# Kernel optimization log

Hardware: AMD Instinct MI355X
Metric: run time of the kernel (lower is better)

## Reference

```python
import jax, jax.numpy as jnp
import numpy as np

N = 50000        # nodes
E = 1600000      # edges (avg degree 32)
DIM_IN = 128
H = 4            # num_heads
D1 = 100         # gc1 per-head out dim
D2 = 20          # gc2 per-head out dim
B = 64           # graphs in the batch
EPS = 1e-5
SLOPE = 0.01     # torch leaky_relu default


def setup_inputs() -> dict:
    key = jax.random.key(0)
    ks = jax.random.split(key, 16)
    sc = lambda fan: 1.0 / np.sqrt(fan)
    inp = {
        'feat': jax.random.normal(ks[0], (N, DIM_IN), jnp.float32),
        'src': jax.random.randint(ks[1], (E,), 0, N, jnp.int32),
        'dst': jax.random.randint(ks[2], (E,), 0, N, jnp.int32),
        'graph_id': jnp.sort(jax.random.randint(ks[3], (N,), 0, B, jnp.int32)),
        # GAT layer 1: per-head fc weight [H, din, dout], attn vector [H, 2*dout]
        'W1': jax.random.normal(ks[4], (H, DIM_IN, D1), jnp.float32) * sc(DIM_IN),
        'a1': jax.random.normal(ks[5], (H, 2 * D1), jnp.float32) * sc(2 * D1),
        # GAT layer 2 (input is cat of heads: H*D1 = 400)
        'W2': jax.random.normal(ks[6], (H, H * D1, D2), jnp.float32) * sc(H * D1),
        'a2': jax.random.normal(ks[7], (H, 2 * D2), jnp.float32) * sc(2 * D2),
        # readout MLP 20 -> 128 -> 32 -> 1
        'Wf1': jax.random.normal(ks[8], (D2, 128), jnp.float32) * sc(D2),
        'bf1': jnp.zeros((128,), jnp.float32),
        'Wf2': jax.random.normal(ks[9], (128, 32), jnp.float32) * sc(128),
        'bf2': jnp.zeros((32,), jnp.float32),
        'Wf3': jax.random.normal(ks[10], (32, 1), jnp.float32) * sc(32),
        'bf3': jnp.zeros((1,), jnp.float32),
        'gamma2': jnp.ones((32,), jnp.float32),   # bn2 weight
        'beta2': jnp.zeros((32,), jnp.float32),   # bn2 bias
    }
    return inp


def _gat_heads(h, W, a, src, dst):
    """Per-head GAT: gather-attn -> segment softmax over dst mailboxes -> scatter-sum.
    Returns list of [N, dout] head outputs. Loop over H=4 heads (small fixed set)."""
    outs = []
    for i in range(W.shape[0]):
        z = h @ W[i]                               # [N, dout]
        d = z.shape[1]
        s_src = z @ a[i, :d]                       # [N] (attn split: a.[z_src,z_dst])
        s_dst = z @ a[i, d:]                       # [N]
        e = jax.nn.leaky_relu(s_src[src] + s_dst[dst], SLOPE)   # [E]
        m = jax.ops.segment_max(e, dst, num_segments=N)          # stable softmax max
        ex = jnp.exp(e - m[dst])
        den = jax.ops.segment_sum(ex, dst, num_segments=N)
        alpha = ex / den[dst]                      # [E] segment softmax
        outs.append(jax.ops.segment_sum(alpha[:, None] * z[src], dst, num_segments=N))
    return outs


def reference(feat, src, dst, graph_id, W1, a1, W2, a2,
              Wf1, bf1, Wf2, bf2, Wf3, bf3, gamma2, beta2):
    src = src.astype(jnp.int32); dst = dst.astype(jnp.int32)
    h = jax.nn.relu(jnp.concatenate(_gat_heads(feat, W1, a1, src, dst), axis=1))  # [N,400]
    h = jax.nn.relu(jnp.mean(jnp.stack(_gat_heads(h, W2, a2, src, dst), 0), 0))   # [N,20]
    # dgl.mean_nodes: per-graph mean of node features
    counts = jax.ops.segment_sum(jnp.ones((N,), h.dtype), graph_id, num_segments=B)
    hg = jax.ops.segment_sum(h, graph_id, num_segments=B) / counts[:, None]        # [B,20]
    out = jax.nn.relu(hg @ Wf1 + bf1)              # dropout = identity (eval)
    out = out @ Wf2 + bf2                          # [B,32]
    mu = jnp.mean(out, axis=0)                     # BatchNorm1d (training stats, biased var)
    var = jnp.mean((out - mu) ** 2, axis=0)
    out = jax.nn.relu(gamma2 * (out - mu) * jax.lax.rsqrt(var + EPS) + beta2)
    return out @ Wf3 + bf3                         # [B,1]
```

## Files before the change

### kernel.cpp

```cpp
#include <hip/hip_runtime.h>
#include <hip/hip_bf16.h>
#include <math.h>

#define N_NODES 50000
#define N_EDGES 1600000
#define DIN 128
#define NH 4
#define D1 100
#define D2 20
#define NB 64
#define EPS_BN 1e-5f


typedef unsigned int uint;
typedef unsigned short ushort;
typedef short short8v __attribute__((ext_vector_type(8)));
typedef float float4v __attribute__((ext_vector_type(4)));

#define Z1_ROWU 208
#define Z1_HU 52
#define Z2_ROWU 64

__device__ __forceinline__ void bf16x2_unpack(uint p, float& lo, float& hi) {
  lo = __uint_as_float(p << 16);
  hi = __uint_as_float(p & 0xffff0000u);
}

__device__ __forceinline__ ushort f2bf(float f) {
  uint u = __float_as_uint(f);
  return (ushort)((u + 0x7fffu + ((u >> 16) & 1u)) >> 16);
}

__global__ void prep_b1t(const float* __restrict__ W1, ushort* __restrict__ B1t) {
  int o = blockIdx.x * 256 + threadIdx.x;
  int h = o >> 14;
  int r = o & 16383;
  int j = r >> 7, k = r & 127;
  float v = (j < D1) ? W1[((size_t)h * DIN + k) * D1 + j] : 0.f;
  B1t[o] = f2bf(v);
}

__global__ void prep_b2t(const float* __restrict__ W2, ushort* __restrict__ B2t) {
  int idx = blockIdx.x * 256 + threadIdx.x;
  if (idx >= 80 * 416) return;
  int c = idx / 416, k = idx - c * 416;
  int h = c / D2, j = c - h * D2;
  float v = (k < NH * D1) ? W2[((size_t)h * (NH * D1) + k) * D2 + j] : 0.f;
  B2t[idx] = f2bf(v);
}

__global__ __launch_bounds__(256) void gemm1_mfma(const float* __restrict__ feat,
                                                  const ushort* __restrict__ B1t,
                                                  const float* __restrict__ a1,
                                                  ushort* __restrict__ z1b,
                                                  float* __restrict__ ssrc,
                                                  float* __restrict__ sdst) {
  __shared__ __align__(16) short Bs[128 * 136];
  __shared__ float asd[2][104];
  const int row0 = blockIdx.x * 128;
  const int h = blockIdx.y;
  const int tid = threadIdx.x;
  {
    const uint* bsrc = reinterpret_cast<const uint*>(B1t + (size_t)h * 16384);
#pragma unroll
    for (int it = 0; it < 32; it++) {
      int idx = tid + it * 256;
      int j = idx >> 6, kk = idx & 63;
      *reinterpret_cast<uint*>(&Bs[j * 136 + kk * 2]) = bsrc[idx];
    }
  }
  if (tid < 208) {
    int which = tid >= 104;
    int cl = which ? tid - 104 : tid;
    asd[which][cl] = (cl < D1) ? a1[h * 2 * D1 + which * D1 + cl] : 0.f;
  }
  const int wv = tid >> 6, lane = tid & 63;
  const int m = lane & 15, q = lane >> 4;
  short8v a[2][4];
#pragma unroll
  for (int mt = 0; mt < 2; mt++) {
    int row = row0 + wv * 32 + mt * 16 + m;
    bool ok = row < N_NODES;
    const float* fr = feat + (size_t)(ok ? row : 0) * DIN;
#pragma unroll
    for (int kq = 0; kq < 4; kq++) {
      short8v s = (short8v){0, 0, 0, 0, 0, 0, 0, 0};
      if (ok) {
        float4 v0 = *reinterpret_cast<const float4*>(fr + kq * 32 + q * 8);
        float4 v1 = *reinterpret_cast<const float4*>(fr + kq * 32 + q * 8 + 4);
        s[0] = (short)f2bf(v0.x); s[1] = (short)f2bf(v0.y);
        s[2] = (short)f2bf(v0.z); s[3] = (short)f2bf(v0.w);
        s[4] = (short)f2bf(v1.x); s[5] = (short)f2bf(v1.y);
        s[6] = (short)f2bf(v1.z); s[7] = (short)f2bf(v1.w);
      }
      a[mt][kq] = s;
    }
  }
  __syncthreads();
  float4v acc[2][8];
#pragma unroll
  for (int mt = 0; mt < 2; mt++)
#pragma unroll
    for (int t = 0; t < 8; t++) acc[mt][t] = (float4v){0.f, 0.f, 0.f, 0.f};
#pragma unroll
  for (int kq = 0; kq < 4; kq++) {
#pragma unroll
    for (int t = 0; t < 8; t++) {
      short8v b = *reinterpret_cast<const short8v*>(&Bs[(t * 16 + m) * 136 + kq * 32 + q * 8]);
      acc[0][t] = __builtin_amdgcn_mfma_f32_16x16x32_bf16(a[0][kq], b, acc[0][t], 0, 0, 0);
      acc[1][t] = __builtin_amdgcn_mfma_f32_16x16x32_bf16(a[1][kq], b, acc[1][t], 0, 0, 0);
    }
  }
#pragma unroll
  for (int mt = 0; mt < 2; mt++) {
#pragma unroll
    for (int t = 0; t < 8; t++) {
      int cl = t * 16 + m;
      if (cl < 104) {
#pragma unroll
        for (int reg = 0; reg < 4; reg++) {
          int row = row0 + wv * 32 + mt * 16 + q * 4 + reg;
          if (row < N_NODES)
            z1b[(size_t)row * 416 + h * 104 + cl] = (cl < D1) ? f2bf(acc[mt][t][reg]) : (ushort)0;
        }
      }
    }
  }
  float aws[8], awd[8];
#pragma unroll
  for (int t = 0; t < 8; t++) {
    aws[t] = asd[0][t * 16 + m];
    awd[t] = asd[1][t * 16 + m];
  }
  float s1[2][4], s2v[2][4];
#pragma unroll
  for (int mt = 0; mt < 2; mt++)
#pragma unroll
    for (int reg = 0; reg < 4; reg++) {
      float p1 = 0.f, p2 = 0.f;
#pragma unroll
      for (int t = 0; t < 8; t++) {
        p1 += acc[mt][t][reg] * aws[t];
        p2 += acc[mt][t][reg] * awd[t];
      }
      s1[mt][reg] = p1;
      s2v[mt][reg] = p2;
    }
#pragma unroll
  for (int mt = 0; mt < 2; mt++)
#pragma unroll
    for (int reg = 0; reg < 4; reg++) {
#pragma unroll
      for (int off = 8; off >= 1; off >>= 1) {
        s1[mt][reg] += __shfl_xor(s1[mt][reg], off);
        s2v[mt][reg] += __shfl_xor(s2v[mt][reg], off);
      }
    }
  if (m == 0) {
#pragma unroll
    for (int mt = 0; mt < 2; mt++)
#pragma unroll
      for (int reg = 0; reg < 4; reg++) {
        int row = row0 + wv * 32 + mt * 16 + q * 4 + reg;
        if (row < N_NODES) ssrc[h * N_NODES + row] = s1[mt][reg];
      }
  } else if (m == 1) {
#pragma unroll
    for (int mt = 0; mt < 2; mt++)
#pragma unroll
      for (int reg = 0; reg < 4; reg++) {
        int row = row0 + wv * 32 + mt * 16 + q * 4 + reg;
        if (row < N_NODES) sdst[h * N_NODES + row] = s2v[mt][reg];
      }
  }
}

__global__ __launch_bounds__(256) void gemm2_mfma(const ushort* __restrict__ h1b,
                                                  const ushort* __restrict__ B2t,
                                                  const float* __restrict__ a2,
                                                  ushort* __restrict__ z2b,
                                                  float* __restrict__ ssrc,
                                                  float* __restrict__ sdst) {
  __shared__ __align__(16) short As[64 * 40];
  __shared__ __align__(16) short Bs[80 * 40];
  __shared__ float awcol[2][4][80];
  const int row0 = blockIdx.x * 64;
  const int tid = threadIdx.x;
  const int wv = tid >> 6, lane = tid & 63;
  const int m = lane & 15, q = lane >> 4;
  const uint* au = reinterpret_cast<const uint*>(h1b);
  const uint* bu = reinterpret_cast<const uint*>(B2t);
  uint* asu = reinterpret_cast<uint*>(As);
  uint* bsu = reinterpret_cast<uint*>(Bs);
  for (int i = tid; i < 640; i += 256) {
    int sc = i / 320;
    int r = i - sc * 320;
    int hh = r / 80, col = r - hh * 80;
    int ch = col / 20;
    awcol[sc][hh][col] = (ch == hh) ? a2[hh * 2 * D2 + sc * D2 + (col - 20 * hh)] : 0.f;
  }
  float4v acc[5];
#pragma unroll
  for (int t = 0; t < 5; t++) acc[t] = (float4v){0.f, 0.f, 0.f, 0.f};
  for (int ch = 0; ch < 13; ch++) {
    int k0u = ch * 16;
    {
      int idx = tid;
#pragma unroll
      for (int it = 0; it < 4; it++, idx += 256) {
        int r = idx >> 4, ku = idx & 15;
        int row = row0 + r;
        uint v = 0;
        if (row < N_NODES && (k0u + ku) < 200) v = au[(size_t)row * 200 + k0u + ku];
        asu[r * 20 + ku] = v;
      }
      idx = tid;
#pragma unroll
      for (int it = 0; it < 5; it++, idx += 256) {
        int c = idx >> 4, ku = idx & 15;
        bsu[c * 20 + ku] = bu[(size_t)c * 208 + k0u + ku];
      }
    }
    __syncthreads();
    short8v a = *reinterpret_cast<const short8v*>(&As[(wv * 16 + m) * 40 + q * 8]);
#pragma unroll
    for (int t = 0; t < 5; t++) {
      short8v b = *reinterpret_cast<const short8v*>(&Bs[(t * 16 + m) * 40 + q * 8]);
      acc[t] = __builtin_amdgcn_mfma_f32_16x16x32_bf16(a, b, acc[t], 0, 0, 0);
    }
    __syncthreads();
  }
#pragma unroll
  for (int t = 0; t < 5; t++) {
    int col = t * 16 + m;
#pragma unroll
    for (int reg = 0; reg < 4; reg++) {
      int row = row0 + wv * 16 + q * 4 + reg;
      if (row < N_NODES) z2b[(size_t)row * 128 + col] = f2bf(acc[t][reg]);
    }
  }
  float w1v[4][5], w2v[4][5];
#pragma unroll
  for (int hh = 0; hh < 4; hh++)
#pragma unroll
    for (int t = 0; t < 5; t++) {
      w1v[hh][t] = awcol[0][hh][t * 16 + m];
      w2v[hh][t] = awcol[1][hh][t * 16 + m];
    }
  float ps[2][4][4];
#pragma unroll
  for (int hh = 0; hh < 4; hh++)
#pragma unroll
    for (int reg = 0; reg < 4; reg++) {
      float p1 = 0.f, p2 = 0.f;
#pragma unroll
      for (int t = 0; t < 5; t++) {
        p1 += acc[t][reg] * w1v[hh][t];
        p2 += acc[t][reg] * w2v[hh][t];
      }
      ps[0][hh][reg] = p1;
      ps[1][hh][reg] = p2;
    }
#pragma unroll
  for (int hh = 0; hh < 4; hh++)
#pragma unroll
    for (int reg = 0; reg < 4; reg++) {
#pragma unroll
      for (int off = 8; off >= 1; off >>= 1) {
        ps[0][hh][reg] += __shfl_xor(ps[0][hh][reg], off);
        ps[1][hh][reg] += __shfl_xor(ps[1][hh][reg], off);
      }
    }
#pragma unroll
  for (int hh = 0; hh < 4; hh++) {
    if (m == hh) {
#pragma unroll
      for (int reg = 0; reg < 4; reg++) {
        int row = row0 + wv * 16 + q * 4 + reg;
        if (row < N_NODES) ssrc[hh * N_NODES + row] = ps[0][hh][reg];
      }
    }
    if (m == hh + 4) {
#pragma unroll
      for (int reg = 0; reg < 4; reg++) {
        int row = row0 + wv * 16 + q * 4 + reg;
        if (row < N_NODES) sdst[hh * N_NODES + row] = ps[1][hh][reg];
      }
    }
  }
}

__global__ void hist_kernel(const int* __restrict__ dst, int* __restrict__ cnt,
                            int* __restrict__ rank) {
  int e = blockIdx.x * blockDim.x + threadIdx.x;
  if (e < N_EDGES) rank[e] = atomicAdd(&cnt[dst[e]], 1);
}

__global__ __launch_bounds__(512) void scan1_kernel(const int* __restrict__ cnt,
                                                    int* __restrict__ row_ptr,
                                                    int* __restrict__ btot, int n) {
  __shared__ int ws[8];
  int b = blockIdx.x, tid = threadIdx.x, lane = tid & 63, wv = tid >> 6;
  int i = b * 512 + tid;
  int v = (i < n) ? cnt[i] : 0;
  int orig = v;
  for (int off = 1; off < 64; off <<= 1) {
    int t = __shfl_up(v, off);
    if (lane >= off) v += t;
  }
  if (lane == 63) ws[wv] = v;
  __syncthreads();
  int wo = 0;
  for (int j = 0; j < wv; j++) wo += ws[j];
  if (i < n) row_ptr[i] = wo + v - orig;
  if (tid == 511) btot[b] = wo + v;
}

__global__ __launch_bounds__(128) void scan2_kernel(int* __restrict__ btot,
                                                    int* __restrict__ row_ptr_n, int nb) {
  __shared__ int ws2[2];
  int tid = threadIdx.x, lane = tid & 63, wv = tid >> 6;
  int v = (tid < nb) ? btot[tid] : 0;
  int orig = v;
  for (int off = 1; off < 64; off <<= 1) {
    int t = __shfl_up(v, off);
    if (lane >= off) v += t;
  }
  if (lane == 63) ws2[wv] = v;
  __syncthreads();
  int wo = (wv == 1) ? ws2[0] : 0;
  if (tid < nb) btot[tid] = wo + v - orig;
  if (tid == nb - 1) *row_ptr_n = wo + v;
}

__global__ __launch_bounds__(512) void scan3_kernel(int* __restrict__ row_ptr,
                                                    const int* __restrict__ btot, int n) {
  int i = blockIdx.x * 512 + threadIdx.x;
  if (i < n) row_ptr[i] += btot[blockIdx.x];
}

__global__ void fill_kernel(const int* __restrict__ src, const int* __restrict__ dst,
                            const int* __restrict__ row_ptr, const int* __restrict__ rank,
                            int* __restrict__ csr_src) {
  int e = blockIdx.x * blockDim.x + threadIdx.x;
  if (e < N_EDGES) csr_src[row_ptr[dst[e]] + rank[e]] = src[e];
}

__global__ __launch_bounds__(256) void agg1_kernel(const ushort* __restrict__ z,
                                                   const float* __restrict__ ssrc,
                                                   const float* __restrict__ sdst,
                                                   const int* __restrict__ row_ptr,
                                                   const int* __restrict__ csr_src,
                                                   ushort* __restrict__ h1b) {
  __shared__ float lw[NH][128];
  const int d = blockIdx.x;
  const int h = threadIdx.x >> 6, lane = threadIdx.x & 63;
  const int beg = row_ptr[d], end = row_ptr[d + 1];
  const int deg = end - beg;
  uint* h1u = reinterpret_cast<uint*>(h1b);
  const size_t ou = (size_t)d * 200 + h * 50 + lane;
  const bool act = lane < D1 / 2;
  if (deg == 0) {
    if (act) h1u[ou] = 0u;
    return;
  }
  const int hN = h * N_NODES;
  const float sd = sdst[hN + d];
  const uint* zb = reinterpret_cast<const uint*>(z);
  const int hco = h * Z1_HU + lane;
  float den = 0.f;
  float aE0 = 0.f, aE1 = 0.f, aE2 = 0.f, aE3 = 0.f;
  float aO0 = 0.f, aO1 = 0.f, aO2 = 0.f, aO3 = 0.f;
  for (int c0 = 0; c0 < deg; c0 += 128) {
    const int cn = min(128, deg - c0);
    const int cb = beg + c0;
    for (int i = lane; i < cn; i += 64) {
      int s = csr_src[cb + i];
      float e = ssrc[hN + s] + sd;
      e = fmaxf(e, 0.01f * e);
      float x = __expf(e);
      lw[h][i] = x;
      den += x;
    }
    if (act) {
      int j = 0;
      for (; j + 8 <= cn; j += 8) {
        int s0 = csr_src[cb + j + 0], s1 = csr_src[cb + j + 1];
        int s2 = csr_src[cb + j + 2], s3 = csr_src[cb + j + 3];
        int s4 = csr_src[cb + j + 4], s5 = csr_src[cb + j + 5];
        int s6 = csr_src[cb + j + 6], s7 = csr_src[cb + j + 7];
        float x0 = lw[h][j + 0], x1 = lw[h][j + 1];
        float x2 = lw[h][j + 2], x3 = lw[h][j + 3];
        float x4 = lw[h][j + 4], x5 = lw[h][j + 5];
        float x6 = lw[h][j + 6], x7 = lw[h][j + 7];
        uint p0 = zb[(size_t)s0 * Z1_ROWU + hco];
        uint p1 = zb[(size_t)s1 * Z1_ROWU + hco];
        uint p2 = zb[(size_t)s2 * Z1_ROWU + hco];
        uint p3 = zb[(size_t)s3 * Z1_ROWU + hco];
        uint p4 = zb[(size_t)s4 * Z1_ROWU + hco];
        uint p5 = zb[(size_t)s5 * Z1_ROWU + hco];
        uint p6 = zb[(size_t)s6 * Z1_ROWU + hco];
        uint p7 = zb[(size_t)s7 * Z1_ROWU + hco];
        float lo, hi;
        bf16x2_unpack(p0, lo, hi); aE0 += x0 * lo; aO0 += x0 * hi;
        bf16x2_unpack(p1, lo, hi); aE1 += x1 * lo; aO1 += x1 * hi;
        bf16x2_unpack(p2, lo, hi); aE2 += x2 * lo; aO2 += x2 * hi;
        bf16x2_unpack(p3, lo, hi); aE3 += x3 * lo; aO3 += x3 * hi;
        bf16x2_unpack(p4, lo, hi); aE0 += x4 * lo; aO0 += x4 * hi;
        bf16x2_unpack(p5, lo, hi); aE1 += x5 * lo; aO1 += x5 * hi;
        bf16x2_unpack(p6, lo, hi); aE2 += x6 * lo; aO2 += x6 * hi;
        bf16x2_unpack(p7, lo, hi); aE3 += x7 * lo; aO3 += x7 * hi;
      }
      for (; j < cn; j++) {
        int s = csr_src[cb + j];
        float x = lw[h][j];
        uint p = zb[(size_t)s * Z1_ROWU + hco];
        float lo, hi;
        bf16x2_unpack(p, lo, hi);
        aE0 += x * lo;
        aO0 += x * hi;
      }
    }
  }
#pragma unroll
  for (int off = 32; off > 0; off >>= 1) den += __shfl_xor(den, off);
  if (!act) return;
  float inv = 1.0f / den;
  float vE = ((aE0 + aE1) + (aE2 + aE3)) * inv;
  float vO = ((aO0 + aO1) + (aO2 + aO3)) * inv;
  vE = vE > 0.f ? vE : 0.f;
  vO = vO > 0.f ? vO : 0.f;
  h1u[ou] = (uint)f2bf(vE) | ((uint)f2bf(vO) << 16);
}

__global__ __launch_bounds__(256) void agg2_kernel(const ushort* __restrict__ z,
                                                   const float* __restrict__ ssrc,
                                                   const float* __restrict__ sdst,
                                                   const int* __restrict__ row_ptr,
                                                   const int* __restrict__ csr_src,
                                                   float* __restrict__ h2) {
  __shared__ float xw[4][8][4];
  __shared__ int sw[4][8];
  __shared__ float accb[4][40][2];
  __shared__ float denb[4][4];
  const int d = blockIdx.x;
  const int wv = threadIdx.x >> 6, lane = threadIdx.x & 63;
  const int beg = row_ptr[d];
  const int deg = row_ptr[d + 1] - beg;
  if (deg == 0) {
    if (threadIdx.x < D2) h2[(size_t)d * D2 + threadIdx.x] = 0.f;
    return;
  }
  const int eh_h = lane & 3, eh_e = lane >> 2;
  const int hq = lane / 10;
  const uint* zu = reinterpret_cast<const uint*>(z);
  float sd = 0.f;
  if (lane < 32) sd = sdst[eh_h * N_NODES + d];
  float den = 0.f;
  float acc0 = 0.f, acc1 = 0.f;
  for (int c0 = wv * 8; c0 < deg; c0 += 32) {
    const int cn = min(8, deg - c0);
    const int cb = beg + c0;
    if (lane < 32) {
      int ee = (eh_e < cn) ? eh_e : 0;
      int s = csr_src[cb + ee];
      float e = ssrc[eh_h * N_NODES + s] + sd;
      e = fmaxf(e, 0.01f * e);
      float x = (eh_e < cn) ? __expf(e) : 0.f;
      den += x;
      xw[wv][eh_e][eh_h] = x;
      if (eh_h == 0) sw[wv][eh_e] = s;
    }
    if (lane < 40) {
#pragma unroll
      for (int e = 0; e < 8; e++) {
        int se = sw[wv][e];
        float xx = xw[wv][e][hq];
        uint p = zu[(size_t)se * Z2_ROWU + lane];
        float lo, hi;
        bf16x2_unpack(p, lo, hi);
        acc0 += xx * lo;
        acc1 += xx * hi;
      }
    }
  }
  den += __shfl_xor(den, 4);
  den += __shfl_xor(den, 8);
  den += __shfl_xor(den, 16);
  if (lane < 4) denb[wv][lane] = den;
  if (lane < 40) {
    accb[wv][lane][0] = acc0;
    accb[wv][lane][1] = acc1;
  }
  __syncthreads();
  if (threadIdx.x < 10) {
    int j = threadIdx.x;
    float vE = 0.f, vO = 0.f;
#pragma unroll
    for (int h = 0; h < 4; h++) {
      float dn = denb[0][h] + denb[1][h] + denb[2][h] + denb[3][h];
      float invd = 1.0f / dn;
      int sl = h * 10 + j;
      float lo = accb[0][sl][0] + accb[1][sl][0] + accb[2][sl][0] + accb[3][sl][0];
      float hi = accb[0][sl][1] + accb[1][sl][1] + accb[2][sl][1] + accb[3][sl][1];
      vE += lo * invd;
      vO += hi * invd;
    }
    vE *= 0.25f;
    vO *= 0.25f;
    h2[(size_t)d * D2 + 2 * j] = vE > 0.f ? vE : 0.f;
    h2[(size_t)d * D2 + 2 * j + 1] = vO > 0.f ? vO : 0.f;
  }
}

__global__ __launch_bounds__(256) void pool_kernel(const float* __restrict__ h2,
                                                   const int* __restrict__ gid,
                                                   float* __restrict__ hg,
                                                   int* __restrict__ gcnt) {
  int wave = threadIdx.x >> 6, lane = threadIdx.x & 63;
  int n = (blockIdx.x * 4 + wave) * 64 + lane;
  bool valid = n < N_NODES;
  int g = gid[valid ? n : (N_NODES - 1)];
  int g0 = __shfl(g, 0), g63 = __shfl(g, 63);
  unsigned long long mask = __ballot(valid);
  if (g0 == g63) {
    if (lane == 0) atomicAdd(&gcnt[g0], (int)__popcll(mask));
#pragma unroll
    for (int c = 0; c < D2; c++) {
      float v = valid ? h2[(size_t)n * D2 + c] : 0.f;
#pragma unroll
      for (int off = 32; off > 0; off >>= 1) v += __shfl_xor(v, off);
      if (lane == 0) atomicAdd(&hg[g0 * D2 + c], v);
    }
  } else if (valid) {
    atomicAdd(&gcnt[g], 1);
    for (int c = 0; c < D2; c++) atomicAdd(&hg[g * D2 + c], h2[(size_t)n * D2 + c]);
  }
}

__global__ __launch_bounds__(256) void head_kernel(const float* __restrict__ hg,
                                                   const int* __restrict__ gcnt,
                                                   const float* __restrict__ Wf1,
                                                   const float* __restrict__ bf1,
                                                   const float* __restrict__ Wf2,
                                                   const float* __restrict__ bf2,
                                                   const float* __restrict__ Wf3,
                                                   const float* __restrict__ bf3,
                                                   const float* __restrict__ gamma,
                                                   const float* __restrict__ beta,
                                                   float* __restrict__ out) {
  __shared__ float X[NB][D2];
  __shared__ float T1[NB][128];
  __shared__ float T2[NB][32];
  __shared__ float scale_s[32], shift_s[32];
  int tid = threadIdx.x;
  for (int i = tid; i < NB * D2; i += 256) {
    int r = i / D2, c = i % D2;
    X[r][c] = hg[i] / (float)gcnt[r];
  }
  __syncthreads();
  for (int i = tid; i < NB * 128; i += 256) {
    int r = i >> 7, c = i & 127;
    float s = bf1[c];
#pragma unroll
    for (int k = 0; k < D2; k++) s += X[r][k] * Wf1[k * 128 + c];
    T1[r][c] = s > 0.f ? s : 0.f;
  }
  __syncthreads();
  for (int i = tid; i < NB * 32; i += 256) {
    int r = i >> 5, c = i & 31;
    float s = bf2[c];
#pragma unroll
    for (int k = 0; k < 128; k++) s += T1[r][k] * Wf2[k * 32 + c];
    T2[r][c] = s;
  }
  __syncthreads();
  if (tid < 32) {
    float mu = 0.f;
    for (int r = 0; r < NB; r++) mu += T2[r][tid];
    mu *= (1.f / NB);
    float var = 0.f;
    for (int r = 0; r < NB; r++) {
      float dv = T2[r][tid] - mu;
      var += dv * dv;
    }
    var *= (1.f / NB);
    float sc = gamma[tid] * rsqrtf(var + EPS_BN);
    scale_s[tid] = sc;
    shift_s[tid] = beta[tid] - mu * sc;
  }
  __syncthreads();
  if (tid < NB) {
    float s = bf3[0];
#pragma unroll
    for (int c = 0; c < 32; c++) {
      float y = scale_s[c] * T2[tid][c] + shift_s[c];
      y = y > 0.f ? y : 0.f;
      s += y * Wf3[c];
    }
    out[tid] = s;
  }
}


extern "C" void kernel_launch(void* const* d_in, const int* in_sizes, int n_in,
                              void* d_out, int out_size, void* d_ws, size_t ws_size,
                              hipStream_t stream) {
  const float* feat = (const float*)d_in[0];
  const int* src = (const int*)d_in[1];
  const int* dst = (const int*)d_in[2];
  const int* gid = (const int*)d_in[3];
  const float* W1 = (const float*)d_in[4];
  const float* a1 = (const float*)d_in[5];
  const float* W2 = (const float*)d_in[6];
  const float* a2 = (const float*)d_in[7];
  const float* Wf1 = (const float*)d_in[8];
  const float* bf1 = (const float*)d_in[9];
  const float* Wf2 = (const float*)d_in[10];
  const float* bf2 = (const float*)d_in[11];
  const float* Wf3 = (const float*)d_in[12];
  const float* bf3 = (const float*)d_in[13];
  const float* gamma2 = (const float*)d_in[14];
  const float* beta2 = (const float*)d_in[15];
  float* outp = (float*)d_out;

  char* p = (char*)d_ws;
  auto alloc = [&](size_t bytes) {
    void* q = (void*)p;
    p += (bytes + 255) & ~(size_t)255;
    return q;
  };
  ushort* z1b = (ushort*)alloc((size_t)N_NODES * 416 * 2);
  ushort* z2b = (ushort*)alloc((size_t)N_NODES * 128 * 2);
  ushort* h1b = (ushort*)alloc((size_t)N_NODES * NH * D1 * 2);
  float* h2 = (float*)alloc((size_t)N_NODES * D2 * 4);
  float* ssrc = (float*)alloc((size_t)NH * N_NODES * 4);
  float* sdst = (float*)alloc((size_t)NH * N_NODES * 4);
  int* cnt = (int*)alloc((size_t)N_NODES * 4);
  int* row_ptr = (int*)alloc((size_t)(N_NODES + 1) * 4);
  int* rank = (int*)alloc((size_t)N_EDGES * 4);
  int* csr = (int*)alloc((size_t)N_EDGES * 4);
  int* btot = (int*)alloc((size_t)128 * 4);
  ushort* B1t = (ushort*)alloc((size_t)NH * 128 * 128 * 2);
  ushort* B2t = (ushort*)alloc((size_t)80 * 416 * 2);
  float* hg = (float*)alloc((size_t)NB * D2 * 4);
  int* gcnt = (int*)alloc((size_t)NB * 4);

  const int rows128 = (N_NODES + 127) / 128;
  const int rows64 = (N_NODES + 63) / 64;
  const int eblk = (N_EDGES + 255) / 256;
  const int nblk = (N_NODES + 255) / 256;
  const int sblk = (N_NODES + 511) / 512;

  hipMemsetAsync(cnt, 0, (size_t)N_NODES * 4, stream);
  hist_kernel<<<eblk, 256, 0, stream>>>(dst, cnt, rank);
  scan1_kernel<<<sblk, 512, 0, stream>>>(cnt, row_ptr, btot, N_NODES);
  scan2_kernel<<<1, 128, 0, stream>>>(btot, row_ptr + N_NODES, sblk);
  scan3_kernel<<<sblk, 512, 0, stream>>>(row_ptr, btot, N_NODES);
  fill_kernel<<<eblk, 256, 0, stream>>>(src, dst, row_ptr, rank, csr);

  prep_b1t<<<256, 256, 0, stream>>>(W1, B1t);
  prep_b2t<<<130, 256, 0, stream>>>(W2, B2t);

  gemm1_mfma<<<dim3(rows128, NH), 256, 0, stream>>>(feat, B1t, a1, z1b, ssrc, sdst);
  agg1_kernel<<<N_NODES, 256, 0, stream>>>(z1b, ssrc, sdst, row_ptr, csr, h1b);

  gemm2_mfma<<<rows64, 256, 0, stream>>>(h1b, B2t, a2, z2b, ssrc, sdst);
  agg2_kernel<<<N_NODES, 256, 0, stream>>>(z2b, ssrc, sdst, row_ptr, csr, h2);

  hipMemsetAsync(hg, 0, (size_t)NB * D2 * 4, stream);
  hipMemsetAsync(gcnt, 0, (size_t)NB * 4, stream);
  pool_kernel<<<nblk, 256, 0, stream>>>(h2, gid, hg, gcnt);
  head_kernel<<<1, 256, 0, stream>>>(hg, gcnt, Wf1, bf1, Wf2, bf2, Wf3, bf3,
                                     gamma2, beta2, outp);
}
```

Baseline: 615.8 us.

## Map one wave per node in agg2 and stage full W2 tile in gemm2

agg2 now gives each destination node to a single wavefront rather than a 256-thread block. Cross-lane shuffles replace the shared-memory staging and the block-wide barrier-based reduction, which should cut idle waves and synchronisation for low-degree nodes. gemm2 loads each wave's A rows straight into registers with vector loads and stages the whole B matrix (about 64KB) in LDS once, removing the per-chunk barriers. The large LDS footprint may lower gemm2 occupancy, and the row-strided B reads in LDS may cause bank conflicts.

```diff
diff --git a/kernel.cpp b/kernel.cpp
--- a/kernel.cpp
+++ b/kernel.cpp
@@ -16,6 +16,7 @@
 typedef unsigned short ushort;
 typedef short short8v __attribute__((ext_vector_type(8)));
 typedef float float4v __attribute__((ext_vector_type(4)));
+typedef uint uint4v __attribute__((ext_vector_type(4)));
 
 #define Z1_ROWU 208
 #define Z1_HU 52
@@ -181,8 +182,7 @@
                                                   ushort* __restrict__ z2b,
                                                   float* __restrict__ ssrc,
                                                   float* __restrict__ sdst) {
-  __shared__ __align__(16) short As[64 * 40];
-  __shared__ __align__(16) short Bs[80 * 40];
+  __shared__ __align__(16) short Bs[80 * 400 + 16];
   __shared__ float awcol[2][4][80];
   const int row0 = blockIdx.x * 64;
   const int tid = threadIdx.x;
@@ -190,8 +190,22 @@
   const int m = lane & 15, q = lane >> 4;
   const uint* au = reinterpret_cast<const uint*>(h1b);
   const uint* bu = reinterpret_cast<const uint*>(B2t);
-  uint* asu = reinterpret_cast<uint*>(As);
   uint* bsu = reinterpret_cast<uint*>(Bs);
+  const int row = row0 + wv * 16 + m;
+  const bool rok = row < N_NODES;
+  uint4v a_all[13];
+#pragma unroll
+  for (int ch = 0; ch < 13; ch++) {
+    int k0 = ch * 16 + q * 4;
+    uint4v v = (uint4v){0u, 0u, 0u, 0u};
+    if (rok && (k0 + 4 <= 200)) v = *reinterpret_cast<const uint4v*>(au + (size_t)row * 200 + k0);
+    a_all[ch] = v;
+  }
+  for (int i = tid; i < 16000; i += 256) {
+    int c = i / 200, k = i - c * 200;
+    bsu[c * 200 + k] = bu[(size_t)c * 208 + k];
+  }
+  if (tid < 8) bsu[16000 + tid] = 0u;
   for (int i = tid; i < 640; i += 256) {
     int sc = i / 320;
     int r = i - sc * 320;
@@ -199,44 +213,26 @@
     int ch = col / 20;
     awcol[sc][hh][col] = (ch == hh) ? a2[hh * 2 * D2 + sc * D2 + (col - 20 * hh)] : 0.f;
   }
+  __syncthreads();
   float4v acc[5];
 #pragma unroll
   for (int t = 0; t < 5; t++) acc[t] = (float4v){0.f, 0.f, 0.f, 0.f};
+#pragma unroll
   for (int ch = 0; ch < 13; ch++) {
-    int k0u = ch * 16;
-    {
-      int idx = tid;
-#pragma unroll
-      for (int it = 0; it < 4; it++, idx += 256) {
-        int r = idx >> 4, ku = idx & 15;
-        int row = row0 + r;
-        uint v = 0;
-        if (row < N_NODES && (k0u + ku) < 200) v = au[(size_t)row * 200 + k0u + ku];
-        asu[r * 20 + ku] = v;
-      }
-      idx = tid;
-#pragma unroll
-      for (int it = 0; it < 5; it++, idx += 256) {
-        int c = idx >> 4, ku = idx & 15;
-        bsu[c * 20 + ku] = bu[(size_t)c * 208 + k0u + ku];
-      }
-    }
-    __syncthreads();
-    short8v a = *reinterpret_cast<const short8v*>(&As[(wv * 16 + m) * 40 + q * 8]);
+    short8v a = *reinterpret_cast<const short8v*>(&a_all[ch]);
 #pragma unroll
     for (int t = 0; t < 5; t++) {
-      short8v b = *reinterpret_cast<const short8v*>(&Bs[(t * 16 + m) * 40 + q * 8]);
+      short8v b = *reinterpret_cast<const short8v*>(&Bs[(t * 16 + m) * 400 + ch * 32 + q * 8]);
       acc[t] = __builtin_amdgcn_mfma_f32_16x16x32_bf16(a, b, acc[t], 0, 0, 0);
     }
-    __syncthreads();
   }
 #pragma unroll
   for (int t = 0; t < 5; t++) {
     int col = t * 16 + m;
 #pragma unroll
     for (int reg = 0; reg < 4; reg++) {
-      int row = row0 + wv * 16 + q * 4 + reg;
-      if (row < N_NODES) z2b[(size_t)row * 128 + col] = f2bf(acc[t][reg]);
+      int r2 = row0 + wv * 16 + q * 4 + reg;
+      if (r2 < N_NODES) z2b[(size_t)r2 * 128 + col] = f2bf(acc[t][reg]);
     }
   }
   float w1v[4][5], w2v[4][5];
@@ -276,15 +272,15 @@
     if (m == hh) {
 #pragma unroll
       for (int reg = 0; reg < 4; reg++) {
-        int row = row0 + wv * 16 + q * 4 + reg;
-        if (row < N_NODES) ssrc[hh * N_NODES + row] = ps[0][hh][reg];
+        int r2 = row0 + wv * 16 + q * 4 + reg;
+        if (r2 < N_NODES) ssrc[hh * N_NODES + r2] = ps[0][hh][reg];
       }
     }
     if (m == hh + 4) {
 #pragma unroll
       for (int reg = 0; reg < 4; reg++) {
-        int row = row0 + wv * 16 + q * 4 + reg;
-        if (row < N_NODES) sdst[hh * N_NODES + row] = ps[1][hh][reg];
+        int r2 = row0 + wv * 16 + q * 4 + reg;
+        if (r2 < N_NODES) sdst[hh * N_NODES + r2] = ps[1][hh][reg];
       }
     }
   }
@@ -439,46 +435,44 @@
                                                    const int* __restrict__ row_ptr,
                                                    const int* __restrict__ csr_src,
                                                    float* __restrict__ h2) {
-  __shared__ float xw[4][8][4];
-  __shared__ int sw[4][8];
-  __shared__ float accb[4][40][2];
-  __shared__ float denb[4][4];
-  const int d = blockIdx.x;
   const int wv = threadIdx.x >> 6, lane = threadIdx.x & 63;
+  const int d = blockIdx.x * 4 + wv;
+  if (d >= N_NODES) return;
   const int beg = row_ptr[d];
   const int deg = row_ptr[d + 1] - beg;
   if (deg == 0) {
-    if (threadIdx.x < D2) h2[(size_t)d * D2 + threadIdx.x] = 0.f;
+    if (lane < 10) {
+      h2[(size_t)d * D2 + 2 * lane] = 0.f;
+      h2[(size_t)d * D2 + 2 * lane + 1] = 0.f;
+    }
     return;
   }
   const int eh_h = lane & 3, eh_e = lane >> 2;
   const int hq = lane / 10;
   const uint* zu = reinterpret_cast<const uint*>(z);
-  float sd = 0.f;
-  if (lane < 32) sd = sdst[eh_h * N_NODES + d];
-  float den = 0.f;
-  float acc0 = 0.f, acc1 = 0.f;
-  for (int c0 = wv * 8; c0 < deg; c0 += 32) {
+  const float sd = (lane < 32) ? sdst[eh_h * N_NODES + d] : 0.f;
+  float den = 0.f, acc0 = 0.f, acc1 = 0.f;
+  for (int c0 = 0; c0 < deg; c0 += 8) {
     const int cn = min(8, deg - c0);
     const int cb = beg + c0;
+    float x = 0.f;
+    int s = 0;
     if (lane < 32) {
       int ee = (eh_e < cn) ? eh_e : 0;
-      int s = csr_src[cb + ee];
+      s = csr_src[cb + ee];
       float e = ssrc[eh_h * N_NODES + s] + sd;
       e = fmaxf(e, 0.01f * e);
-      float x = (eh_e < cn) ? __expf(e) : 0.f;
+      x = (eh_e < cn) ? __expf(e) : 0.f;
       den += x;
-      xw[wv][eh_e][eh_h] = x;
-      if (eh_h == 0) sw[wv][eh_e] = s;
-    }
-    if (lane < 40) {
-#pragma unroll
-      for (int e = 0; e < 8; e++) {
-        int se = sw[wv][e];
-        float xx = xw[wv][e][hq];
-        uint p = zu[(size_t)se * Z2_ROWU + lane];
+    }
+#pragma unroll
+    for (int e = 0; e < 8; e++) {
+      float xx = __shfl(x, e * 4 + hq);
+      int se = __shfl(s, e * 4);
+      if (lane < 40) {
+        uint pd = zu[(size_t)se * Z2_ROWU + lane];
         float lo, hi;
-        bf16x2_unpack(p, lo, hi);
+        bf16x2_unpack(pd, lo, hi);
         acc0 += xx * lo;
         acc1 += xx * hi;
       }
@@ -487,29 +481,21 @@
   den += __shfl_xor(den, 4);
   den += __shfl_xor(den, 8);
   den += __shfl_xor(den, 16);
-  if (lane < 4) denb[wv][lane] = den;
-  if (lane < 40) {
-    accb[wv][lane][0] = acc0;
-    accb[wv][lane][1] = acc1;
-  }
-  __syncthreads();
-  if (threadIdx.x < 10) {
-    int j = threadIdx.x;
-    float vE = 0.f, vO = 0.f;
-#pragma unroll
-    for (int h = 0; h < 4; h++) {
-      float dn = denb[0][h] + denb[1][h] + denb[2][h] + denb[3][h];
-      float invd = 1.0f / dn;
-      int sl = h * 10 + j;
-      float lo = accb[0][sl][0] + accb[1][sl][0] + accb[2][sl][0] + accb[3][sl][0];
-      float hi = accb[0][sl][1] + accb[1][sl][1] + accb[2][sl][1] + accb[3][sl][1];
-      vE += lo * invd;
-      vO += hi * invd;
-    }
-    vE *= 0.25f;
-    vO *= 0.25f;
-    h2[(size_t)d * D2 + 2 * j] = vE > 0.f ? vE : 0.f;
-    h2[(size_t)d * D2 + 2 * j + 1] = vO > 0.f ? vO : 0.f;
+  float dh = __shfl(den, hq);
+  float invd = 1.0f / dh;
+  float v0 = acc0 * invd, v1 = acc1 * invd;
+  const int j10 = (lane < 10) ? lane : 0;
+  float s0 = 0.f, s1 = 0.f;
+#pragma unroll
+  for (int k = 0; k < 4; k++) {
+    s0 += __shfl(v0, j10 + 10 * k);
+    s1 += __shfl(v1, j10 + 10 * k);
+  }
+  if (lane < 10) {
+    s0 *= 0.25f;
+    s1 *= 0.25f;
+    h2[(size_t)d * D2 + 2 * lane] = s0 > 0.f ? s0 : 0.f;
+    h2[(size_t)d * D2 + 2 * lane + 1] = s1 > 0.f ? s1 : 0.f;
   }
 }
 
@@ -650,6 +636,7 @@
   const int rows64 = (N_NODES + 63) / 64;
   const int eblk = (N_EDGES + 255) / 256;
   const int nblk = (N_NODES + 255) / 256;
+  const int dblk4 = (N_NODES + 3) / 4;
   const int sblk = (N_NODES + 511) / 512;
 
   hipMemsetAsync(cnt, 0, (size_t)N_NODES * 4, stream);
@@ -666,7 +653,7 @@
   agg1_kernel<<<N_NODES, 256, 0, stream>>>(z1b, ssrc, sdst, row_ptr, csr, h1b);
 
   gemm2_mfma<<<rows64, 256, 0, stream>>>(h1b, B2t, a2, z2b, ssrc, sdst);
-  agg2_kernel<<<N_NODES, 256, 0, stream>>>(z2b, ssrc, sdst, row_ptr, csr, h2);
+  agg2_kernel<<<dblk4, 256, 0, stream>>>(z2b, ssrc, sdst, row_ptr, csr, h2);
 
   hipMemsetAsync(hg, 0, (size_t)NB * D2 * 4, stream);
   hipMemsetAsync(gcnt, 0, (size_t)NB * 4, stream);
```

After: 659.4 us. +7.1%, slower.
